# Performance work log

Hardware: AMD Instinct MI355X
Metric: run time of the kernel (lower is better)

Reference implementation:

```python
import jax, jax.numpy as jnp
import numpy as np

# Hyperparameters from init_kwargs
MIN_STREAK_HIGH = 4
MIN_STREAK_LOW = 7
MIN_STREAKS_HIGH_ACT = 2
MIN_STREAKS_LOW_ACT = 3
HIGH_IMPACT_INIT = 0.18
LOW_IMPACT_INIT = 0.05
MAX_ADJUST = 0.35
HIGH_DECAY = 0.5
LOW_DECAY = 0.5

B, T = 16384, 4096


def setup_inputs() -> dict:
    key = jax.random.key(0)
    k1, k2 = jax.random.split(key)
    drowsiness_index = jax.random.uniform(k1, (B, 1), dtype=jnp.float32)
    gesture_sequence = jax.random.randint(k2, (B, T, 1), 0, 3, dtype=jnp.int32)
    return {"drowsiness_index": drowsiness_index, "gesture_sequence": gesture_sequence}


def _adjustments(gesture_sequence):
    # [B, T] yawning mask (gesture class 2)
    m = jnp.squeeze(gesture_sequence, axis=-1) == 2
    Tn = m.shape[1]
    r = jnp.arange(Tn, dtype=jnp.int32)  # [T]
    # Vectorized run-length encoding: index of most recent non-yawning frame.
    # reset[b, t] = t where m==False, else -1; running max gives last reset position.
    reset = jnp.where(m, jnp.int32(-1), r[None, :])  # [B, T]
    last_reset = jax.lax.cummax(reset, axis=1)  # [B, T]
    cnt = jnp.where(m, r[None, :] - last_reset, 0)  # streak length so far at t
    # A streak ends at t if m[t] and (t is last or m[t+1] is False).
    next_m = jnp.concatenate([m[:, 1:], jnp.zeros((m.shape[0], 1), dtype=bool)], axis=1)
    is_end = m & ~next_m  # [B, T]
    high_count = jnp.sum(is_end & (cnt >= MIN_STREAK_HIGH), axis=1)  # [B] int32
    low_count = jnp.sum(is_end & (cnt >= MIN_STREAK_LOW), axis=1)
    high_adj = HIGH_IMPACT_INIT * jnp.exp(
        -HIGH_DECAY * (high_count - MIN_STREAKS_HIGH_ACT).astype(jnp.float32))
    high_adj = jnp.where(high_count >= MIN_STREAKS_HIGH_ACT, high_adj, 0.0)
    low_adj = LOW_IMPACT_INIT * jnp.exp(
        -LOW_DECAY * (low_count - MIN_STREAKS_LOW_ACT).astype(jnp.float32))
    low_adj = jnp.where(low_count >= MIN_STREAKS_LOW_ACT, low_adj, 0.0)
    total = jnp.minimum(high_adj + low_adj, MAX_ADJUST)  # [B]
    return total[:, None]  # [B, 1]


def reference(drowsiness_index, gesture_sequence):
    adj = _adjustments(gesture_sequence)
    return jnp.clip(drowsiness_index + adj, 0.0, 1.0)
```

## Files before the change

### kernel.cpp

```cpp
#include <hip/hip_runtime.h>
#include <stdint.h>


#define NROWS 16384
#define TLEN  4096

__global__ __launch_bounds__(256, 4) void yawn_adjust_kernel(
    const float* __restrict__ drows,
    const int* __restrict__ gest,
    float* __restrict__ out)
{
    const int lane = threadIdx.x & 63;
    const int row  = blockIdx.x * 4 + (threadIdx.x >> 6);
    if (row >= NROWS) return;

    const int* gp = gest + (size_t)row * TLEN + lane;

    uint32_t mlo = 0u, mhi = 0u;
    #pragma unroll
    for (int j0 = 0; j0 < 64; j0 += 16) {
        int v[16];
        #pragma unroll
        for (int k = 0; k < 16; ++k)
            v[k] = gp[(j0 + k) * 64];
        #pragma unroll
        for (int k = 0; k < 16; ++k) {
            unsigned long long b = __ballot(v[k] == 2);
            if (lane == j0 + k) {
                mlo = (uint32_t)b;
                mhi = (uint32_t)(b >> 32);
            }
        }
    }

    uint64_t m  = ((uint64_t)mhi << 32) | (uint64_t)mlo;
    bool     full = (m == ~0ull);
    uint64_t nm = ~m;
    int lead  = full ? 64 : (int)__builtin_ctzll(nm);
    int trail = full ? 64 : (int)__builtin_clzll(nm);

    int leadc  = full ? 0 : lead;
    int trailc = full ? 0 : trail;
    uint64_t mi = full ? 0ull : m;
    mi = (mi >> leadc) << leadc;
    mi = (mi << trailc) >> trailc;

    uint64_t w = mi & (mi >> 1);
    w &= (w >> 2);
    int ch = __builtin_popcountll(w & ~(w << 1));
    uint64_t w7 = w & (w >> 3);
    int cl = __builtin_popcountll(w7 & ~(w7 << 1));

    #pragma unroll
    for (int off = 1, len = 64; off < 64; off <<= 1, len <<= 1) {
        int bch    = __shfl_down(ch,    (unsigned)off, 64);
        int bcl    = __shfl_down(cl,    (unsigned)off, 64);
        int blead  = __shfl_down(lead,  (unsigned)off, 64);
        int btrail = __shfl_down(trail, (unsigned)off, 64);

        bool afull = (lead  == len);
        bool bfull = (blead == len);
        int junction = trail + blead;
        bool interior = (!afull) && (!bfull);
        ch += bch + ((interior && junction >= 4) ? 1 : 0);
        cl += bcl + ((interior && junction >= 7) ? 1 : 0);
        lead  = afull ? (len + blead)  : lead;
        trail = bfull ? (len + trail)  : btrail;
    }

    if (lane == 0) {
        int hc, lc;
        if (lead == TLEN) {
            hc = 1; lc = 1;
        } else {
            hc = ch + (lead >= 4 ? 1 : 0) + (trail >= 4 ? 1 : 0);
            lc = cl + (lead >= 7 ? 1 : 0) + (trail >= 7 ? 1 : 0);
        }
        float hadj = (hc >= 2) ? 0.18f * expf(-0.5f * (float)(hc - 2)) : 0.0f;
        float ladj = (lc >= 3) ? 0.05f * expf(-0.5f * (float)(lc - 3)) : 0.0f;
        float tot  = fminf(hadj + ladj, 0.35f);
        float r    = drows[row] + tot;
        out[row]   = fminf(fmaxf(r, 0.0f), 1.0f);
    }
}

extern "C" void kernel_launch(void* const* d_in, const int* in_sizes, int n_in,
                              void* d_out, int out_size, void* d_ws, size_t ws_size,
                              hipStream_t stream) {
    (void)in_sizes; (void)n_in; (void)d_ws; (void)ws_size; (void)out_size;
    const float* drows = (const float*)d_in[0];
    const int*   gest  = (const int*)d_in[1];
    float*       out   = (float*)d_out;
    dim3 grid(NROWS / 4);
    yawn_adjust_kernel<<<grid, 256, 0, stream>>>(drows, gest, out);
}
```

Before: 354.1 us.

## Load gestures as uint4 vectors, transpose through swizzled LDS to build per-lane masks

Each wave now reads its row with 16-byte vector loads, covering the row in two 2048-element halves. Each half is staged through a swizzled LDS buffer so that every lane can build a 32-bit yawn mask over contiguous frames. This replaces the 64 strided 4-byte loads and the 64 ballots per lane used before. The two halves are reduced separately with the shuffle tree and then merged at the junction, which adds LDS traffic and a second shuffle reduction in exchange for wider global loads.

```diff
diff --git a/kernel.cpp b/kernel.cpp
--- a/kernel.cpp
+++ b/kernel.cpp
@@ -5,54 +5,30 @@
 #define NROWS 16384
 #define TLEN  4096
 
-__global__ __launch_bounds__(256, 4) void yawn_adjust_kernel(
-    const float* __restrict__ drows,
-    const int* __restrict__ gest,
-    float* __restrict__ out)
+__device__ __forceinline__ int swz(int idx) { return idx ^ ((idx >> 4) & 15); }
+
+__device__ __forceinline__ void leaf_tree(uint32_t m,
+                                          int& ch, int& cl, int& lead, int& trail)
 {
-    const int lane = threadIdx.x & 63;
-    const int row  = blockIdx.x * 4 + (threadIdx.x >> 6);
-    if (row >= NROWS) return;
+    bool full  = (m == 0xFFFFFFFFu);
+    uint32_t nm = ~m;
+    lead  = full ? 32 : __builtin_ctz(nm);
+    trail = full ? 32 : __builtin_clz(nm);
 
-    const int* gp = gest + (size_t)row * TLEN + lane;
+    int lc = full ? 0 : lead;
+    int tc = full ? 0 : trail;
+    uint32_t mi = full ? 0u : m;
+    mi = (mi >> lc) << lc;
+    mi = (mi << tc) >> tc;
 
-    uint32_t mlo = 0u, mhi = 0u;
-    #pragma unroll
-    for (int j0 = 0; j0 < 64; j0 += 16) {
-        int v[16];
-        #pragma unroll
-        for (int k = 0; k < 16; ++k)
-            v[k] = gp[(j0 + k) * 64];
-        #pragma unroll
-        for (int k = 0; k < 16; ++k) {
-            unsigned long long b = __ballot(v[k] == 2);
-            if (lane == j0 + k) {
-                mlo = (uint32_t)b;
-                mhi = (uint32_t)(b >> 32);
-            }
-        }
-    }
-
-    uint64_t m  = ((uint64_t)mhi << 32) | (uint64_t)mlo;
-    bool     full = (m == ~0ull);
-    uint64_t nm = ~m;
-    int lead  = full ? 64 : (int)__builtin_ctzll(nm);
-    int trail = full ? 64 : (int)__builtin_clzll(nm);
-
-    int leadc  = full ? 0 : lead;
-    int trailc = full ? 0 : trail;
-    uint64_t mi = full ? 0ull : m;
-    mi = (mi >> leadc) << leadc;
-    mi = (mi << trailc) >> trailc;
-
-    uint64_t w = mi & (mi >> 1);
+    uint32_t w = mi & (mi >> 1);
     w &= (w >> 2);
-    int ch = __builtin_popcountll(w & ~(w << 1));
-    uint64_t w7 = w & (w >> 3);
-    int cl = __builtin_popcountll(w7 & ~(w7 << 1));
+    ch = __builtin_popcount(w & ~(w << 1));
+    uint32_t w7 = w & (w >> 3);
+    cl = __builtin_popcount(w7 & ~(w7 << 1));
 
     #pragma unroll
-    for (int off = 1, len = 64; off < 64; off <<= 1, len <<= 1) {
+    for (int off = 1, len = 32; off < 64; off <<= 1, len <<= 1) {
         int bch    = __shfl_down(ch,    (unsigned)off, 64);
         int bcl    = __shfl_down(cl,    (unsigned)off, 64);
         int blead  = __shfl_down(lead,  (unsigned)off, 64);
@@ -64,9 +40,63 @@
         bool interior = (!afull) && (!bfull);
         ch += bch + ((interior && junction >= 4) ? 1 : 0);
         cl += bcl + ((interior && junction >= 7) ? 1 : 0);
-        lead  = afull ? (len + blead)  : lead;
-        trail = bfull ? (len + trail)  : btrail;
+        lead  = afull ? (len + blead) : lead;
+        trail = bfull ? (len + trail) : btrail;
     }
+}
+
+__device__ __forceinline__ uint32_t build_mask(const uint4* buf, int lane)
+{
+    uint32_t m = 0;
+    #pragma unroll
+    for (int j = 0; j < 8; ++j) {
+        uint4 q = buf[swz(lane * 8 + j)];
+        uint32_t nib = (q.x == 2 ? 1u : 0u) | (q.y == 2 ? 2u : 0u)
+                     | (q.z == 2 ? 4u : 0u) | (q.w == 2 ? 8u : 0u);
+        m |= nib << (4 * j);
+    }
+    return m;
+}
+
+__global__ __launch_bounds__(256, 4) void yawn_adjust_kernel(
+    const float* __restrict__ drows,
+    const int* __restrict__ gest,
+    float* __restrict__ out)
+{
+    __shared__ uint4 lds[4][512];
+    const int lane = threadIdx.x & 63;
+    const int wid  = (int)(threadIdx.x >> 6);
+    const int row  = blockIdx.x * 4 + wid;
+    uint4* buf = lds[wid];
+
+    const uint4* g4 = (const uint4*)gest + (size_t)row * (TLEN / 4);
+
+    uint4 a[8], b[8];
+    #pragma unroll
+    for (int c = 0; c < 8; ++c) a[c] = g4[c * 64 + lane];
+    #pragma unroll
+    for (int c = 0; c < 8; ++c) b[c] = g4[512 + c * 64 + lane];
+
+    #pragma unroll
+    for (int c = 0; c < 8; ++c) buf[swz(c * 64 + lane)] = a[c];
+    uint32_t m0 = build_mask(buf, lane);
+    int ch0, cl0, lead0, trail0;
+    leaf_tree(m0, ch0, cl0, lead0, trail0);
+
+    #pragma unroll
+    for (int c = 0; c < 8; ++c) buf[swz(c * 64 + lane)] = b[c];
+    uint32_t m1 = build_mask(buf, lane);
+    int ch1, cl1, lead1, trail1;
+    leaf_tree(m1, ch1, cl1, lead1, trail1);
+
+    bool afull = (lead0 == 2048);
+    bool bfull = (lead1 == 2048);
+    int junction = trail0 + lead1;
+    bool interior = (!afull) && (!bfull);
+    int ch = ch0 + ch1 + ((interior && junction >= 4) ? 1 : 0);
+    int cl = cl0 + cl1 + ((interior && junction >= 7) ? 1 : 0);
+    int lead  = afull ? (2048 + lead1)  : lead0;
+    int trail = bfull ? (2048 + trail0) : trail1;
 
     if (lane == 0) {
         int hc, lc;
```

Result: no change. 357.0 us (+0.8%).
